# Kernel tuning notes

Hardware: AMD Instinct MI355X
Metric: run time of the kernel (lower is better)

Reference implementation:

```python
import jax, jax.numpy as jnp
import numpy as np

SCALE_POS = 2.0
SCALE_NEG = 50.0
THRESH = 0.7
MARGIN = 0.1
GAMMA = 0.3
EPS = 1e-5       # epsilon excluding self / near-duplicate positives
COS_EPS = 1e-8   # torch CosineSimilarity eps


def setup_inputs() -> dict:
    key = jax.random.key(0)
    k1, k2 = jax.random.split(key)
    B, D, C = 4096, 128, 256
    emb = jax.random.normal(k1, (B, D), dtype=jnp.float32)
    emb = emb / jnp.linalg.norm(emb, axis=1, keepdims=True)  # metric-learning embeddings are L2-normalized
    labels = jax.random.randint(k2, (B,), 0, C)
    return {"embeddings": emb, "labels": labels}


def reference(embeddings, labels):
    B = embeddings.shape[0]
    sim = embeddings @ embeddings.T                                   # [B,B]
    same = labels[:, None] == labels[None, :]
    pos_mask = same & (sim < 1.0 - EPS)
    neg_mask = ~same
    inf = jnp.inf
    min_pos = jnp.min(jnp.where(pos_mask, sim, inf), axis=1)          # [B] min(pos_pair_)
    max_neg = jnp.max(jnp.where(neg_mask, sim, -inf), axis=1)         # [B] max(neg_pair_)
    neg_keep = neg_mask & (sim + MARGIN > min_pos[:, None])           # mined negatives
    pos_keep = pos_mask & (sim - MARGIN < max_neg[:, None])           # mined positives
    valid = jnp.any(neg_keep, axis=1) & jnp.any(pos_keep, axis=1)
    # hardest positive index per anchor (argmin over kept positives; first-min tie-break like torch)
    j = jnp.argmin(jnp.where(pos_keep, sim, inf), axis=1)             # [B]
    d_p = embeddings[j] - embeddings                                  # f_p - f_a, [B,D]
    # dot[i,n] = (e_n - e_i) . d_p[i]
    dot = jnp.einsum('nd,id->in', embeddings, d_p) \
        - jnp.einsum('id,id->i', embeddings, d_p)[:, None]            # [B,B]
    sq = jnp.sum(embeddings * embeddings, axis=1)                     # [B]
    # ||e_n - e_i|| via Gram matrix; clamp avoids inf grad of sqrt at the diagonal (masked anyway)
    norm_n = jnp.sqrt(jnp.maximum(sq[None, :] + sq[:, None] - 2.0 * sim, 1e-12))
    norm_p = jnp.linalg.norm(d_p, axis=1)                             # [B] ||f_p - f_a||
    denom = jnp.maximum(norm_n, COS_EPS) * jnp.maximum(norm_p, COS_EPS)[:, None]
    reg = GAMMA * dot / denom                                         # [B,B] gamma * cos(f_n-f_a, f_p-f_a)
    pos_terms = jnp.where(pos_keep, jnp.exp(-SCALE_POS * (sim - THRESH)), 0.0)
    neg_terms = jnp.where(neg_keep, jnp.exp(SCALE_NEG * (sim - THRESH - reg)), 0.0)
    pos_loss = jnp.log1p(jnp.sum(pos_terms, axis=1)) / SCALE_POS
    neg_loss = jnp.log1p(jnp.sum(neg_terms, axis=1)) / SCALE_NEG
    row_loss = jnp.where(valid, pos_loss + neg_loss, 0.0)
    return jnp.sum(row_loss) / B
```

## Files before the change

### kernel.cpp

```cpp
#include <hip/hip_runtime.h>
#include <math.h>

#define NB 4096

#define SCALE_POS 2.0f
#define SCALE_NEG 50.0f
#define THRESH    0.7f
#define MARGIN    0.1f
#define GAMMA     0.3f
#define EPS_SELF  1e-5f

typedef __attribute__((ext_vector_type(8))) short s16x8;
typedef __attribute__((ext_vector_type(16))) float f32x16;
typedef unsigned long long u64;
typedef unsigned int u32;
typedef unsigned char u8;

__device__ __forceinline__ short f2bf(float x) {
  u32 u = __float_as_uint(x);
  return (short)((u + 0x7FFFu + ((u >> 16) & 1u)) >> 16);
}
__device__ __forceinline__ float bf2f(short h) {
  return __uint_as_float(((u32)(unsigned short)h) << 16);
}
__device__ __forceinline__ u32 mono16(u32 h) {
  return (h & 0x8000u) ? (h ^ 0xFFFFu) : (h | 0x8000u);
}
__device__ __forceinline__ float unmono16(u32 m) {
  u32 h = (m & 0x8000u) ? (m & 0x7FFFu) : (~m & 0xFFFFu);
  return bf2f((short)h);
}

__global__ __launch_bounds__(256) void k1_convert(
    const float* __restrict__ emb, const int* __restrict__ labels,
    short* __restrict__ F, u8* __restrict__ labu8) {
  int t = blockIdx.x * 256 + threadIdx.x;
  int T = t >> 9, s = (t >> 6) & 7, l = t & 63;
  int row = T * 32 + (l & 31);
  int c4 = s * 4 + (l >> 5) * 2;
  const float4* e4 = (const float4*)emb;
  float4 v0 = e4[row * 32 + c4];
  float4 v1 = e4[row * 32 + c4 + 1];
  float xs[8] = {v0.x, v0.y, v0.z, v0.w, v1.x, v1.y, v1.z, v1.w};
  s16x8 h, lo;
#pragma unroll
  for (int e = 0; e < 8; ++e) {
    short hh = f2bf(xs[e]);
    h[e] = hh;
    lo[e] = f2bf(xs[e] - bf2f(hh));
  }
  ((s16x8*)F)[(T * 16 + s) * 64 + l] = h;
  ((s16x8*)F)[(T * 16 + 8 + s) * 64 + l] = lo;
  if (t < 1024) {
    int4 lb = ((const int4*)labels)[t];
    uchar4 p;
    p.x = (u8)lb.x; p.y = (u8)lb.y; p.z = (u8)lb.z; p.w = (u8)lb.w;
    ((uchar4*)labu8)[t] = p;
  }
}

__global__ __launch_bounds__(256, 4) void k2_pass1(
    const short* __restrict__ F, short* __restrict__ simh) {
  int tid = threadIdx.x, w = tid >> 6, l = tid & 63;
  int lo5 = l & 31, hi = l >> 5;
  int mt0 = blockIdx.y * 4 + (w >> 1) * 2;
  int nt0 = blockIdx.x * 4 + (w & 1) * 2;
  const s16x8* F8 = (const s16x8*)F;

  f32x16 acc[2][2] = {};
#pragma unroll 1
  for (int s = 0; s < 8; ++s) {
    s16x8 ah[2], al[2], bh[2], bl[2];
#pragma unroll
    for (int t = 0; t < 2; ++t) {
      int ia = ((mt0 + t) * 16 + s) * 64 + l;
      int ib = ((nt0 + t) * 16 + s) * 64 + l;
      ah[t] = F8[ia]; al[t] = F8[ia + 512];
      bh[t] = F8[ib]; bl[t] = F8[ib + 512];
    }
#pragma unroll
    for (int ti = 0; ti < 2; ++ti)
#pragma unroll
      for (int tj = 0; tj < 2; ++tj) {
        acc[ti][tj] = __builtin_amdgcn_mfma_f32_32x32x16_bf16(ah[ti], bh[tj], acc[ti][tj], 0, 0, 0);
        acc[ti][tj] = __builtin_amdgcn_mfma_f32_32x32x16_bf16(ah[ti], bl[tj], acc[ti][tj], 0, 0, 0);
        acc[ti][tj] = __builtin_amdgcn_mfma_f32_32x32x16_bf16(al[ti], bh[tj], acc[ti][tj], 0, 0, 0);
      }
  }

#pragma unroll
  for (int ti = 0; ti < 2; ++ti)
#pragma unroll
    for (int tj = 0; tj < 2; ++tj) {
      int n = (nt0 + tj) * 32 + lo5;
#pragma unroll
      for (int q = 0; q < 4; ++q)
#pragma unroll
        for (int rr = 0; rr < 4; ++rr) {
          int m = (mt0 + ti) * 32 + q * 8 + hi * 4 + rr;
          simh[(size_t)m * NB + n] = f2bf(acc[ti][tj][q * 4 + rr]);
        }
    }
}

__global__ __launch_bounds__(256) void k4_row(
    const short* __restrict__ simh, const u8* __restrict__ labu8,
    float* __restrict__ rowloss) {
  int i = blockIdx.x, tid = threadIdx.x;
  int lm = (int)labu8[i];
  const s16x8* sI = (const s16x8*)(simh + (size_t)i * NB);
  const u64* L8 = (const u64*)labu8;
  s16x8 a0 = sI[tid], a1 = sI[tid + 256];
  u64 lb0 = L8[tid], lb1 = L8[tid + 256];

  u32 pk = 0xFFFFFFFFu;
  u32 nk = 0u;
  {
    s16x8 aa[2] = {a0, a1};
    u64 ll[2] = {lb0, lb1};
#pragma unroll
    for (int c = 0; c < 2; ++c) {
      int nbase = (tid + c * 256) * 8;
#pragma unroll
      for (int e = 0; e < 8; ++e) {
        u32 h = (u32)(unsigned short)aa[c][e];
        u32 key = (mono16(h) << 16) | (u32)(nbase + e);
        int ln = (int)((ll[c] >> (8 * e)) & 255u);
        float s = bf2f((short)h);
        if (ln == lm) {
          if (s < 1.0f - EPS_SELF) pk = pk < key ? pk : key;
        } else {
          nk = nk > key ? nk : key;
        }
      }
    }
  }
#pragma unroll
  for (int d = 1; d < 64; d <<= 1) {
    u32 po = __shfl_xor(pk, d, 64); pk = pk < po ? pk : po;
    u32 no = __shfl_xor(nk, d, 64); nk = nk > no ? nk : no;
  }
  __shared__ u32 spk[4], snk[4];
  __shared__ float s_mp, s_mx, s_dpp, s_inpp;
  __shared__ int s_j, s_valid;
  if ((tid & 63) == 0) { spk[tid >> 6] = pk; snk[tid >> 6] = nk; }
  __syncthreads();
  if (tid == 0) {
    u32 P = spk[0], N = snk[0];
#pragma unroll
    for (int q = 1; q < 4; ++q) {
      P = P < spk[q] ? P : spk[q];
      N = N > snk[q] ? N : snk[q];
    }
    float minpos = unmono16(P >> 16);
    float maxneg = unmono16(N >> 16);
    bool valid = (maxneg + MARGIN > minpos);
    s_valid = valid ? 1 : 0;
    s_j = valid ? (int)(P & 0xFFFFu) : i;
    s_mp = minpos;
    s_mx = maxneg;
    s_dpp = minpos - 1.0f;
    s_inpp = 1.0f / fmaxf(sqrtf(fmaxf(2.0f - 2.0f * minpos, 1e-12f)), 1e-8f);
  }
  __syncthreads();
  if (!s_valid) {
    if (tid == 0) rowloss[i] = 0.0f;
    return;
  }
  float mp = s_mp, mx = s_mx, dpp = s_dpp, inpp = s_inpp;
  const s16x8* sJ = (const s16x8*)(simh + (size_t)s_j * NB);
  s16x8 b0 = sJ[tid], b1 = sJ[tid + 256];

  float ps = 0.0f, ns = 0.0f;
  {
    s16x8 aa[2] = {a0, a1};
    s16x8 bb[2] = {b0, b1};
    u64 ll[2] = {lb0, lb1};
#pragma unroll
    for (int c = 0; c < 2; ++c) {
#pragma unroll
      for (int e = 0; e < 8; ++e) {
        float s = bf2f(aa[c][e]);
        int ln = (int)((ll[c] >> (8 * e)) & 255u);
        if (ln == lm) {
          if (s < 1.0f - EPS_SELF && s - MARGIN < mx)
            ps += __expf(-SCALE_POS * (s - THRESH));
        } else if (s + MARGIN > mp) {
          float sjv = bf2f(bb[c][e]);
          float nn = fmaxf(sqrtf(fmaxf(2.0f - 2.0f * s, 1e-12f)), 1e-8f);
          float rg = GAMMA * (sjv - s - dpp) * inpp * __builtin_amdgcn_rcpf(nn);
          ns += __expf(SCALE_NEG * (s - THRESH - rg));
        }
      }
    }
  }
#pragma unroll
  for (int d = 1; d < 64; d <<= 1) {
    ps += __shfl_xor(ps, d, 64);
    ns += __shfl_xor(ns, d, 64);
  }
  __shared__ float redp[4], redn[4];
  if ((tid & 63) == 0) {
    redp[tid >> 6] = ps;
    redn[tid >> 6] = ns;
  }
  __syncthreads();
  if (tid == 0) {
    float tp = redp[0] + redp[1] + redp[2] + redp[3];
    float tn = redn[0] + redn[1] + redn[2] + redn[3];
    rowloss[i] = log1pf(tp) * (1.0f / SCALE_POS) + log1pf(tn) * (1.0f / SCALE_NEG);
  }
}

__global__ __launch_bounds__(1024) void k5_final(
    const float* __restrict__ rowloss, float* __restrict__ out) {
  int tid = threadIdx.x;
  float local = 0.0f;
  for (int r = tid; r < NB; r += 1024) local += rowloss[r];
#pragma unroll
  for (int d = 1; d < 64; d <<= 1) local += __shfl_xor(local, d, 64);
  __shared__ float partial[16];
  if ((tid & 63) == 0) partial[tid >> 6] = local;
  __syncthreads();
  if (tid == 0) {
    float t = 0.0f;
#pragma unroll
    for (int q = 0; q < 16; ++q) t += partial[q];
    out[0] = t / (float)NB;
  }
}

extern "C" void kernel_launch(void* const* d_in, const int* in_sizes, int n_in,
                              void* d_out, int out_size, void* d_ws, size_t ws_size,
                              hipStream_t stream) {
  const float* emb = (const float*)d_in[0];
  const int* labels = (const int*)d_in[1];
  float* out = (float*)d_out;
  char* ws = (char*)d_ws;

  short* simh = (short*)ws;
  short* F = (short*)(ws + ((size_t)NB * NB * 2));
  char* base = ws + ((size_t)NB * NB * 2) + (2 << 20);
  float* rowloss = (float*)(base);
  u8* labu8 = (u8*)(base + 16384);

  hipLaunchKernelGGL(k1_convert, dim3(256), dim3(256), 0, stream,
                     emb, labels, F, labu8);
  hipLaunchKernelGGL(k2_pass1, dim3(NB / 128, NB / 128), dim3(256), 0, stream,
                     F, simh);
  hipLaunchKernelGGL(k4_row, dim3(NB), dim3(256), 0, stream,
                     simh, labu8, rowloss);
  hipLaunchKernelGGL(k5_final, dim3(1), dim3(1024), 0, stream, rowloss, out);
}
```

Before: 56.13 us.

## Fold final reduction into row kernel via atomics and reshape GEMM block tiling

Removes the separate final-reduction kernel. Each valid row now atomically adds its scaled loss into the output, which the convert kernel zeroes first. The similarity GEMM's block tile also changes from 128x128 (2x2 waves) to 64x256 (1x4 waves). This saves one kernel launch, but adds 4096 float atomics on one address, makes the summation order nondeterministic, and changes operand reuse in the GEMM.

After: 91.37 us. 1.63x slower.

```diff
diff --git a/kernel.cpp b/kernel.cpp
--- a/kernel.cpp
+++ b/kernel.cpp
@@ -33,7 +33,7 @@
 
 __global__ __launch_bounds__(256) void k1_convert(
     const float* __restrict__ emb, const int* __restrict__ labels,
-    short* __restrict__ F, u8* __restrict__ labu8) {
+    short* __restrict__ F, u8* __restrict__ labu8, float* __restrict__ out) {
   int t = blockIdx.x * 256 + threadIdx.x;
   int T = t >> 9, s = (t >> 6) & 7, l = t & 63;
   int row = T * 32 + (l & 31);
@@ -57,14 +57,15 @@
     p.x = (u8)lb.x; p.y = (u8)lb.y; p.z = (u8)lb.z; p.w = (u8)lb.w;
     ((uchar4*)labu8)[t] = p;
   }
+  if (t == 0) out[0] = 0.0f;
 }
 
 __global__ __launch_bounds__(256, 4) void k2_pass1(
     const short* __restrict__ F, short* __restrict__ simh) {
   int tid = threadIdx.x, w = tid >> 6, l = tid & 63;
   int lo5 = l & 31, hi = l >> 5;
-  int mt0 = blockIdx.y * 4 + (w >> 1) * 2;
-  int nt0 = blockIdx.x * 4 + (w & 1) * 2;
+  int mt0 = blockIdx.y * 2;
+  int nt0 = blockIdx.x * 8 + w * 2;
   const s16x8* F8 = (const s16x8*)F;
 
   f32x16 acc[2][2] = {};
@@ -105,7 +106,7 @@
 
 __global__ __launch_bounds__(256) void k4_row(
     const short* __restrict__ simh, const u8* __restrict__ labu8,
-    float* __restrict__ rowloss) {
+    float* __restrict__ out) {
   int i = blockIdx.x, tid = threadIdx.x;
   int lm = (int)labu8[i];
   const s16x8* sI = (const s16x8*)(simh + (size_t)i * NB);
@@ -163,10 +164,7 @@
     s_inpp = 1.0f / fmaxf(sqrtf(fmaxf(2.0f - 2.0f * minpos, 1e-12f)), 1e-8f);
   }
   __syncthreads();
-  if (!s_valid) {
-    if (tid == 0) rowloss[i] = 0.0f;
-    return;
-  }
+  if (!s_valid) return;
   float mp = s_mp, mx = s_mx, dpp = s_dpp, inpp = s_inpp;
   const s16x8* sJ = (const s16x8*)(simh + (size_t)s_j * NB);
   s16x8 b0 = sJ[tid], b1 = sJ[tid + 256];
@@ -208,25 +206,8 @@
   if (tid == 0) {
     float tp = redp[0] + redp[1] + redp[2] + redp[3];
     float tn = redn[0] + redn[1] + redn[2] + redn[3];
-    rowloss[i] = log1pf(tp) * (1.0f / SCALE_POS) + log1pf(tn) * (1.0f / SCALE_NEG);
-  }
-}
-
-__global__ __launch_bounds__(1024) void k5_final(
-    const float* __restrict__ rowloss, float* __restrict__ out) {
-  int tid = threadIdx.x;
-  float local = 0.0f;
-  for (int r = tid; r < NB; r += 1024) local += rowloss[r];
-#pragma unroll
-  for (int d = 1; d < 64; d <<= 1) local += __shfl_xor(local, d, 64);
-  __shared__ float partial[16];
-  if ((tid & 63) == 0) partial[tid >> 6] = local;
-  __syncthreads();
-  if (tid == 0) {
-    float t = 0.0f;
-#pragma unroll
-    for (int q = 0; q < 16; ++q) t += partial[q];
-    out[0] = t / (float)NB;
+    float rl = log1pf(tp) * (1.0f / SCALE_POS) + log1pf(tn) * (1.0f / SCALE_NEG);
+    atomicAdd(out, rl * (1.0f / (float)NB));
   }
 }
 
@@ -240,15 +221,12 @@
 
   short* simh = (short*)ws;
   short* F = (short*)(ws + ((size_t)NB * NB * 2));
-  char* base = ws + ((size_t)NB * NB * 2) + (2 << 20);
-  float* rowloss = (float*)(base);
-  u8* labu8 = (u8*)(base + 16384);
+  u8* labu8 = (u8*)(ws + ((size_t)NB * NB * 2) + (2 << 20));
 
   hipLaunchKernelGGL(k1_convert, dim3(256), dim3(256), 0, stream,
-                     emb, labels, F, labu8);
-  hipLaunchKernelGGL(k2_pass1, dim3(NB / 128, NB / 128), dim3(256), 0, stream,
+                     emb, labels, F, labu8, out);
+  hipLaunchKernelGGL(k2_pass1, dim3(NB / 256, NB / 64), dim3(256), 0, stream,
                      F, simh);
   hipLaunchKernelGGL(k4_row, dim3(NB), dim3(256), 0, stream,
-                     simh, labu8, rowloss);
-  hipLaunchKernelGGL(k5_final, dim3(1), dim3(1024), 0, stream, rowloss, out);
-}
+                     simh, labu8, out);
+}
```

## Assign one wavefront per row in row kernel and reshape GEMM block tiles

Applied to the files above, without the earlier changes.

The row-loss kernel now processes one row per 64-lane wavefront, with four rows per block, instead of one row per 256-thread block. This removes the shared-memory reductions and __syncthreads barriers. It also caches the positive-label mask in a 64-bit bitmask so labels are not re-decoded in the second pass. Each lane now holds 8 chunks of sim values and labels in registers, which raises register pressure. Separately, the similarity GEMM block is reshaped from a 4x4 to a 2x8 arrangement of 32x32 tiles, changing which A/B tiles are shared across waves.

Result: slower. 61.56 us (+9.7%).

```diff
diff --git a/kernel.cpp b/kernel.cpp
--- a/kernel.cpp
+++ b/kernel.cpp
@@ -63,8 +63,8 @@
     const short* __restrict__ F, short* __restrict__ simh) {
   int tid = threadIdx.x, w = tid >> 6, l = tid & 63;
   int lo5 = l & 31, hi = l >> 5;
-  int mt0 = blockIdx.y * 4 + (w >> 1) * 2;
-  int nt0 = blockIdx.x * 4 + (w & 1) * 2;
+  int mt0 = blockIdx.y * 2;
+  int nt0 = blockIdx.x * 8 + w * 2;
   const s16x8* F8 = (const s16x8*)F;
 
   f32x16 acc[2][2] = {};
@@ -106,32 +106,36 @@
 __global__ __launch_bounds__(256) void k4_row(
     const short* __restrict__ simh, const u8* __restrict__ labu8,
     float* __restrict__ rowloss) {
-  int i = blockIdx.x, tid = threadIdx.x;
+  int w = threadIdx.x >> 6, l = threadIdx.x & 63;
+  int i = blockIdx.x * 4 + w;
   int lm = (int)labu8[i];
   const s16x8* sI = (const s16x8*)(simh + (size_t)i * NB);
   const u64* L8 = (const u64*)labu8;
-  s16x8 a0 = sI[tid], a1 = sI[tid + 256];
-  u64 lb0 = L8[tid], lb1 = L8[tid + 256];
+
+  s16x8 a[8];
+  u64 lab[8];
+#pragma unroll
+  for (int ch = 0; ch < 8; ++ch) a[ch] = sI[ch * 64 + l];
+#pragma unroll
+  for (int ch = 0; ch < 8; ++ch) lab[ch] = L8[ch * 64 + l];
 
   u32 pk = 0xFFFFFFFFu;
   u32 nk = 0u;
-  {
-    s16x8 aa[2] = {a0, a1};
-    u64 ll[2] = {lb0, lb1};
-#pragma unroll
-    for (int c = 0; c < 2; ++c) {
-      int nbase = (tid + c * 256) * 8;
-#pragma unroll
-      for (int e = 0; e < 8; ++e) {
-        u32 h = (u32)(unsigned short)aa[c][e];
-        u32 key = (mono16(h) << 16) | (u32)(nbase + e);
-        int ln = (int)((ll[c] >> (8 * e)) & 255u);
+  u64 posm = 0ull;
+#pragma unroll
+  for (int ch = 0; ch < 8; ++ch) {
+    int nb = (ch * 64 + l) * 8;
+#pragma unroll
+    for (int e = 0; e < 8; ++e) {
+      u32 h = (u32)(unsigned short)a[ch][e];
+      u32 key = (mono16(h) << 16) | (u32)(nb + e);
+      int ln = (int)((lab[ch] >> (8 * e)) & 255u);
+      if (ln == lm) {
+        posm |= (1ull << (ch * 8 + e));
         float s = bf2f((short)h);
-        if (ln == lm) {
-          if (s < 1.0f - EPS_SELF) pk = pk < key ? pk : key;
-        } else {
-          nk = nk > key ? nk : key;
-        }
+        if (s < 1.0f - EPS_SELF) pk = pk < key ? pk : key;
+      } else {
+        nk = nk > key ? nk : key;
       }
     }
   }
@@ -140,57 +144,37 @@
     u32 po = __shfl_xor(pk, d, 64); pk = pk < po ? pk : po;
     u32 no = __shfl_xor(nk, d, 64); nk = nk > no ? nk : no;
   }
-  __shared__ u32 spk[4], snk[4];
-  __shared__ float s_mp, s_mx, s_dpp, s_inpp;
-  __shared__ int s_j, s_valid;
-  if ((tid & 63) == 0) { spk[tid >> 6] = pk; snk[tid >> 6] = nk; }
-  __syncthreads();
-  if (tid == 0) {
-    u32 P = spk[0], N = snk[0];
-#pragma unroll
-    for (int q = 1; q < 4; ++q) {
-      P = P < spk[q] ? P : spk[q];
-      N = N > snk[q] ? N : snk[q];
-    }
-    float minpos = unmono16(P >> 16);
-    float maxneg = unmono16(N >> 16);
-    bool valid = (maxneg + MARGIN > minpos);
-    s_valid = valid ? 1 : 0;
-    s_j = valid ? (int)(P & 0xFFFFu) : i;
-    s_mp = minpos;
-    s_mx = maxneg;
-    s_dpp = minpos - 1.0f;
-    s_inpp = 1.0f / fmaxf(sqrtf(fmaxf(2.0f - 2.0f * minpos, 1e-12f)), 1e-8f);
-  }
-  __syncthreads();
-  if (!s_valid) {
-    if (tid == 0) rowloss[i] = 0.0f;
+  float minpos = unmono16(pk >> 16);
+  float maxneg = unmono16(nk >> 16);
+  bool valid = (maxneg + MARGIN > minpos);
+  if (!valid) {
+    if (l == 0) rowloss[i] = 0.0f;
     return;
   }
-  float mp = s_mp, mx = s_mx, dpp = s_dpp, inpp = s_inpp;
-  const s16x8* sJ = (const s16x8*)(simh + (size_t)s_j * NB);
-  s16x8 b0 = sJ[tid], b1 = sJ[tid + 256];
+  int j = (int)(pk & 0xFFFFu);
+  float mp = minpos, mx = maxneg;
+  float dpp = minpos - 1.0f;
+  float inpp = 1.0f / fmaxf(sqrtf(fmaxf(2.0f - 2.0f * minpos, 1e-12f)), 1e-8f);
+
+  const s16x8* sJ = (const s16x8*)(simh + (size_t)j * NB);
+  s16x8 b[8];
+#pragma unroll
+  for (int ch = 0; ch < 8; ++ch) b[ch] = sJ[ch * 64 + l];
 
   float ps = 0.0f, ns = 0.0f;
-  {
-    s16x8 aa[2] = {a0, a1};
-    s16x8 bb[2] = {b0, b1};
-    u64 ll[2] = {lb0, lb1};
-#pragma unroll
-    for (int c = 0; c < 2; ++c) {
-#pragma unroll
-      for (int e = 0; e < 8; ++e) {
-        float s = bf2f(aa[c][e]);
-        int ln = (int)((ll[c] >> (8 * e)) & 255u);
-        if (ln == lm) {
-          if (s < 1.0f - EPS_SELF && s - MARGIN < mx)
-            ps += __expf(-SCALE_POS * (s - THRESH));
-        } else if (s + MARGIN > mp) {
-          float sjv = bf2f(bb[c][e]);
-          float nn = fmaxf(sqrtf(fmaxf(2.0f - 2.0f * s, 1e-12f)), 1e-8f);
-          float rg = GAMMA * (sjv - s - dpp) * inpp * __builtin_amdgcn_rcpf(nn);
-          ns += __expf(SCALE_NEG * (s - THRESH - rg));
-        }
+#pragma unroll
+  for (int ch = 0; ch < 8; ++ch) {
+#pragma unroll
+    for (int e = 0; e < 8; ++e) {
+      float s = bf2f(a[ch][e]);
+      if ((posm >> (ch * 8 + e)) & 1ull) {
+        if (s < 1.0f - EPS_SELF && s - MARGIN < mx)
+          ps += __expf(-SCALE_POS * (s - THRESH));
+      } else if (s + MARGIN > mp) {
+        float sjv = bf2f(b[ch][e]);
+        float nn = fmaxf(sqrtf(fmaxf(2.0f - 2.0f * s, 1e-12f)), 1e-8f);
+        float rg = GAMMA * (sjv - s - dpp) * inpp * __builtin_amdgcn_rcpf(nn);
+        ns += __expf(SCALE_NEG * (s - THRESH - rg));
       }
     }
   }
@@ -199,17 +183,8 @@
     ps += __shfl_xor(ps, d, 64);
     ns += __shfl_xor(ns, d, 64);
   }
-  __shared__ float redp[4], redn[4];
-  if ((tid & 63) == 0) {
-    redp[tid >> 6] = ps;
-    redn[tid >> 6] = ns;
-  }
-  __syncthreads();
-  if (tid == 0) {
-    float tp = redp[0] + redp[1] + redp[2] + redp[3];
-    float tn = redn[0] + redn[1] + redn[2] + redn[3];
-    rowloss[i] = log1pf(tp) * (1.0f / SCALE_POS) + log1pf(tn) * (1.0f / SCALE_NEG);
-  }
+  if (l == 0)
+    rowloss[i] = log1pf(ps) * (1.0f / SCALE_POS) + log1pf(ns) * (1.0f / SCALE_NEG);
 }
 
 __global__ __launch_bounds__(1024) void k5_final(
@@ -246,9 +221,9 @@
 
   hipLaunchKernelGGL(k1_convert, dim3(256), dim3(256), 0, stream,
                      emb, labels, F, labu8);
-  hipLaunchKernelGGL(k2_pass1, dim3(NB / 128, NB / 128), dim3(256), 0, stream,
+  hipLaunchKernelGGL(k2_pass1, dim3(NB / 256, NB / 64), dim3(256), 0, stream,
                      F, simh);
-  hipLaunchKernelGGL(k4_row, dim3(NB), dim3(256), 0, stream,
+  hipLaunchKernelGGL(k4_row, dim3(NB / 4), dim3(256), 0, stream,
                      simh, labu8, rowloss);
   hipLaunchKernelGGL(k5_final, dim3(1), dim3(1024), 0, stream, rowloss, out);
 }
```
